# Performance work log

Measured on AMD Instinct MI355X. Metric: run time of the kernel, lower is better.

Reference implementation:

```python
import jax, jax.numpy as jnp
import numpy as np

N_CELLS = 2048
D_IN = 512
D_HID = 1024
D_OUT = 512
SYNC = 0.15
DEBATE = 0.15
N_FACTIONS = 8


def setup_inputs() -> dict:
    key = jax.random.key(0)
    ks = jax.random.split(key, 24)
    def w(k, shape, s=0.02):
        return jax.random.normal(k, shape, dtype=jnp.float32) * s
    ein = D_IN + D_HID          # complex-engine input dim (1536)
    gin = D_OUT + 1 + D_HID     # GRU gate input dim (1537)
    return {
        "x": jax.random.normal(ks[0], (1, D_IN), dtype=jnp.float32),
        "h_re": w(ks[1], (N_CELLS, D_HID), 0.1),
        "h_im": w(ks[2], (N_CELLS, D_HID), 0.1),
        "ea_wr": w(ks[3], (ein, D_OUT)), "ea_br": w(ks[4], (D_OUT,)),
        "ea_wi": w(ks[5], (ein, D_OUT)), "ea_bi": w(ks[6], (D_OUT,)),
        "eg_wr": w(ks[7], (ein, D_OUT)), "eg_br": w(ks[8], (D_OUT,)),
        "eg_wi": w(ks[9], (ein, D_OUT)), "eg_bi": w(ks[10], (D_OUT,)),
        "gz_w": w(ks[11], (gin, D_HID)), "gz_b": w(ks[12], (D_HID,)),
        "gr_w": w(ks[13], (gin, D_HID)), "gr_b": w(ks[14], (D_HID,)),
        "ghr_w": w(ks[15], (gin, D_HID)), "ghr_b": w(ks[16], (D_HID,)),
        "ghi_w": w(ks[17], (gin, D_HID)), "ghi_b": w(ks[18], (D_HID,)),
        "oh_w": w(ks[19], (2 * D_OUT, D_IN)), "oh_b": w(ks[20], (D_IN,)),
        "step": 7,
    }


def _clin(a, b, Wr, br, Wi, bi):
    # complex linear: (Wr + iWi)(a + ib) with torch's bias semantics
    return (a @ Wr + br) - (b @ Wi + bi), (b @ Wr + br) + (a @ Wi + bi)


def reference(x, h_re, h_im, ea_wr, ea_br, ea_wi, ea_bi, eg_wr, eg_br, eg_wi, eg_bi,
              gz_w, gz_b, gr_w, gr_b, ghr_w, ghr_b, ghi_w, ghi_b, oh_w, oh_b, step):
    # batch the 256-cell Python loop into single GEMMs over the cell axis
    xb = jnp.broadcast_to(x, (N_CELLS, D_IN))
    c_re = jnp.concatenate([xb, h_re], -1)                       # [N, D_IN+D_HID]
    c_im = jnp.concatenate([jnp.zeros_like(xb), h_im], -1)
    a_re, a_im = _clin(c_re, c_im, ea_wr, ea_br, ea_wi, ea_bi)
    g_re, g_im = _clin(c_re, c_im, eg_wr, eg_br, eg_wi, eg_bi)
    o_re, o_im = a_re - g_re, a_im - g_im                        # [N, D_OUT]
    tension = jnp.mean(o_re**2 + o_im**2, -1)                    # [N]

    # GRU memory update (detached input, matching output.detach())
    so_re = jax.lax.stop_gradient(o_re)
    so_im = jax.lax.stop_gradient(o_im)
    t_sg = jax.lax.stop_gradient(tension)
    mem_re = jnp.concatenate([so_re, t_sg[:, None]], -1)         # [N, D_OUT+1]
    mem_im = jnp.concatenate([so_im, jnp.zeros((N_CELLS, 1), o_im.dtype)], -1)
    x_mag = jnp.sqrt(mem_re**2 + mem_im**2)
    h_mag = jnp.sqrt(h_re**2 + h_im**2)
    cm = jnp.concatenate([x_mag, h_mag], -1)                     # [N, D_OUT+1+D_HID]
    z = jax.nn.sigmoid(cm @ gz_w + gz_b)
    r = jax.nn.sigmoid(cm @ gr_w + gr_b)
    comb_r = jnp.concatenate([mem_re, r * h_re], -1)
    comb_i = jnp.concatenate([mem_im, r * h_im], -1)
    cand_re = jnp.tanh(comb_r @ ghr_w + ghr_b)
    cand_im = jnp.tanh(comb_i @ ghi_w + ghi_b)
    nh_re = jax.lax.stop_gradient((1 - z) * h_re + z * cand_re)
    nh_im = jax.lax.stop_gradient((1 - z) * h_im + z * cand_im)

    # faction sync + debate (linear op, applied per component)
    fs = N_CELLS // N_FACTIONS
    def sync(h):
        hf = h.reshape(N_FACTIONS, fs, D_HID)
        hf = (1 - SYNC) * hf + SYNC * jnp.mean(hf, 1, keepdims=True)
        if step > 5:
            glob = jnp.mean(jnp.mean(hf, 1), 0)                  # [D_HID]
            dc = max(1, fs // 4)
            hf = hf.at[:, :dc].set((1 - DEBATE) * hf[:, :dc] + DEBATE * glob)
        return hf.reshape(N_CELLS, D_HID)
    nh_re, nh_im = sync(nh_re), sync(nh_im)

    # tension-softmax-weighted combination (weights are non-differentiable, .item() in torch)
    w_soft = jax.nn.softmax(t_sg)                                # [N]
    comb_re = (w_soft[:, None] * o_re).sum(0, keepdims=True)     # [1, D_OUT]
    comb_im = (w_soft[:, None] * o_im).sum(0, keepdims=True)
    out_real = jnp.concatenate([comb_re, comb_im], -1)           # [1, 2*D_OUT]
    pred = out_real @ oh_w + oh_b                                # [1, D_IN]
    return pred, jnp.mean(tension), nh_re, nh_im
```

## Files before the change

### kernel.cpp

```cpp
#include <hip/hip_runtime.h>
#include <math.h>

#define N_CELLS 2048
#define D_IN 512
#define D_HID 1024
#define D_OUT 512

typedef __attribute__((ext_vector_type(8))) short bf16x8;
typedef __attribute__((ext_vector_type(4))) float f32x4;
typedef __attribute__((ext_vector_type(4))) short short4v;

#define MFMA16(a, b, c) __builtin_amdgcn_mfma_f32_16x16x32_bf16(a, b, c, 0, 0, 0)

__device__ __forceinline__ short f2bf(float f) {
  union { float f; unsigned u; } v; v.f = f;
  unsigned r = (v.u + 0x7FFFu + ((v.u >> 16) & 1u)) >> 16;
  return (short)r;
}

__device__ __forceinline__ void gl_lds16(const void* g, void* l) {
  __builtin_amdgcn_global_load_lds(
      (const __attribute__((address_space(1))) void*)g,
      (__attribute__((address_space(3))) void*)l, 16, 0, 0);
}

__global__ __launch_bounds__(256) void k_transpose_all(
    const float* __restrict__ w0, const float* __restrict__ w1,
    const float* __restrict__ w2, const float* __restrict__ w3,
    short* __restrict__ t0, short* __restrict__ t1,
    short* __restrict__ t2, short* __restrict__ t3,
    const float* __restrict__ ea_wr, const float* __restrict__ eg_wr,
    const float* __restrict__ ea_wi, const float* __restrict__ eg_wi,
    short* __restrict__ wdrT, short* __restrict__ wdiT, short* __restrict__ wdnT) {
  const int k0 = blockIdx.x * 32, n0 = blockIdx.y * 32;
  const int c = threadIdx.x & 31, r4 = threadIdx.x >> 5;
  if (blockIdx.z < 4) {
    const float* w = (blockIdx.z == 0) ? w0 : (blockIdx.z == 1) ? w1
                   : (blockIdx.z == 2) ? w2 : w3;
    short* wT = (blockIdx.z == 0) ? t0 : (blockIdx.z == 1) ? t1
              : (blockIdx.z == 2) ? t2 : t3;
    __shared__ float t[32][33];
#pragma unroll
    for (int i = 0; i < 4; ++i) {
      int kl = r4 * 4 + i;
      int k = k0 + kl;
      int srcrow = (k < 512) ? k : k + 1;
      t[kl][c] = w[(size_t)srcrow * D_HID + n0 + c];
    }
    __syncthreads();
#pragma unroll
    for (int i = 0; i < 4; ++i) {
      int nl = r4 * 4 + i;
      wT[(size_t)(n0 + nl) * 1536 + k0 + c] = f2bf(t[c][nl]);
    }
  } else {
    if (blockIdx.x >= 32 || blockIdx.y >= 16) return;
    __shared__ float tr[32][33], ti[32][33];
#pragma unroll
    for (int i = 0; i < 4; ++i) {
      int kl = r4 * 4 + i;
      int src = (512 + k0 + kl) * D_OUT + n0 + c;
      tr[kl][c] = ea_wr[src] - eg_wr[src];
      ti[kl][c] = ea_wi[src] - eg_wi[src];
    }
    __syncthreads();
#pragma unroll
    for (int i = 0; i < 4; ++i) {
      int nl = r4 * 4 + i;
      int dst = (n0 + nl) * D_HID + k0 + c;
      float dr = tr[c][nl], di = ti[c][nl];
      wdrT[dst] = f2bf(dr);
      wdiT[dst] = f2bf(di);
      wdnT[dst] = f2bf(-di);
    }
  }
}

__global__ __launch_bounds__(256) void k_prep_h(
    const float* __restrict__ h_re, const float* __restrict__ h_im,
    short* __restrict__ hbre, short* __restrict__ hbim, short* __restrict__ gatesA,
    float* __restrict__ tens) {
  if (threadIdx.x == 0) tens[blockIdx.x] = 0.f;
  int idx4 = (blockIdx.x * 256 + threadIdx.x) * 4;
  int m = idx4 >> 10, n = idx4 & 1023;
  float4 hr = *(const float4*)&h_re[idx4];
  float4 hi = *(const float4*)&h_im[idx4];
  short4v br, bi, bm;
  br.x = f2bf(hr.x); br.y = f2bf(hr.y); br.z = f2bf(hr.z); br.w = f2bf(hr.w);
  bi.x = f2bf(hi.x); bi.y = f2bf(hi.y); bi.z = f2bf(hi.z); bi.w = f2bf(hi.w);
  bm.x = f2bf(sqrtf(hr.x * hr.x + hi.x * hi.x));
  bm.y = f2bf(sqrtf(hr.y * hr.y + hi.y * hi.y));
  bm.z = f2bf(sqrtf(hr.z * hr.z + hi.z * hi.z));
  bm.w = f2bf(sqrtf(hr.w * hr.w + hi.w * hi.w));
  *(short4v*)&hbre[idx4] = br;
  *(short4v*)&hbim[idx4] = bi;
  *(short4v*)&gatesA[(size_t)m * 1536 + 512 + n] = bm;
}

__global__ __launch_bounds__(256) void k_bias_part(
    const float* __restrict__ x,
    const float* __restrict__ ea_wr, const float* __restrict__ ea_wi,
    const float* __restrict__ eg_wr, const float* __restrict__ eg_wi,
    float* __restrict__ bpartr, float* __restrict__ bparti) {
  int n = blockIdx.x * 256 + threadIdx.x;
  int kc = blockIdx.y;
  float sr = 0.f, si = 0.f;
  for (int i = 0; i < 64; ++i) {
    int k = kc * 64 + i;
    float xv = x[k];
    int idx = k * D_OUT + n;
    sr += xv * (ea_wr[idx] - eg_wr[idx]);
    si += xv * (ea_wi[idx] - eg_wi[idx]);
  }
  bpartr[kc * D_OUT + n] = sr;
  bparti[kc * D_OUT + n] = si;
}

__global__ __launch_bounds__(256) void k_bias_red(
    const float* __restrict__ bpartr, const float* __restrict__ bparti,
    const float* __restrict__ ea_br, const float* __restrict__ ea_bi,
    const float* __restrict__ eg_br, const float* __restrict__ eg_bi,
    float* __restrict__ bias_re, float* __restrict__ bias_im) {
  int n = blockIdx.x * 256 + threadIdx.x;
  float sr = 0.f, si = 0.f;
#pragma unroll
  for (int kc = 0; kc < 8; ++kc) { sr += bpartr[kc * D_OUT + n]; si += bparti[kc * D_OUT + n]; }
  float brd = ea_br[n] - eg_br[n];
  float bid = ea_bi[n] - eg_bi[n];
  bias_re[n] = sr + brd - bid;
  bias_im[n] = si + brd + bid;
}

__global__ __launch_bounds__(256) void k_engine(
    const short* __restrict__ hbre, const short* __restrict__ hbim,
    const short* __restrict__ wdrT, const short* __restrict__ wdiT,
    const short* __restrict__ wdnT,
    const float* __restrict__ bias_re, const float* __restrict__ bias_im,
    float* __restrict__ ore, float* __restrict__ oim,
    short* __restrict__ gatesA, short* __restrict__ candAre, short* __restrict__ candAim,
    float* __restrict__ tens) {
  __shared__ short Ar[2 * 64 * 32], Ai[2 * 64 * 32];
  __shared__ short Brs[2 * 32 * 32], Bis[2 * 32 * 32], Bns[2 * 32 * 32];
  const int m0 = blockIdx.x * 64, n0 = blockIdx.y * 32;
  const int tid = threadIdx.x;
  const int wid = tid >> 6, lane = tid & 63;
  const int quad = lane >> 4, lcol = lane & 15;
  const int wm = wid * 16;
  f32x4 accre[2], accim[2];
#pragma unroll
  for (int nt = 0; nt < 2; ++nt) {
    accre[nt] = (f32x4){0.f, 0.f, 0.f, 0.f};
    accim[nt] = (f32x4){0.f, 0.f, 0.f, 0.f};
  }
  for (int k0 = 0; k0 < D_HID; k0 += 64) {
    if (k0) __syncthreads();
#pragma unroll
    for (int i = 0; i < 2; ++i) {
      int c = i * 256 + tid;
      int kh = c >> 8, row = (c >> 2) & 63, kq = c & 3;
      size_t g = (size_t)(m0 + row) * D_HID + k0 + kh * 32 + kq * 8;
      gl_lds16(hbre + g, &Ar[c * 8]);
      gl_lds16(hbim + g, &Ai[c * 8]);
    }
    {
      int c = tid;
      int kh = c >> 7, row = (c >> 2) & 31, kq = c & 3;
      size_t g = (size_t)(n0 + row) * D_HID + k0 + kh * 32 + kq * 8;
      gl_lds16(wdrT + g, &Brs[c * 8]);
      gl_lds16(wdiT + g, &Bis[c * 8]);
      gl_lds16(wdnT + g, &Bns[c * 8]);
    }
    __syncthreads();
#pragma unroll
    for (int kh = 0; kh < 2; ++kh) {
      bf16x8 ar, ai, br[2], bi[2], bn[2];
      int aoff = kh * 2048 + (wm + lcol) * 32 + quad * 8;
      ar = *(const bf16x8*)&Ar[aoff];
      ai = *(const bf16x8*)&Ai[aoff];
#pragma unroll
      for (int nt = 0; nt < 2; ++nt) {
        int boff = kh * 1024 + (nt * 16 + lcol) * 32 + quad * 8;
        br[nt] = *(const bf16x8*)&Brs[boff];
        bi[nt] = *(const bf16x8*)&Bis[boff];
        bn[nt] = *(const bf16x8*)&Bns[boff];
      }
#pragma unroll
      for (int nt = 0; nt < 2; ++nt) {
        accre[nt] = MFMA16(ar, br[nt], accre[nt]);
        accre[nt] = MFMA16(ai, bn[nt], accre[nt]);
        accim[nt] = MFMA16(ar, bi[nt], accim[nt]);
        accim[nt] = MFMA16(ai, br[nt], accim[nt]);
      }
    }
  }
#pragma unroll
  for (int r = 0; r < 4; ++r) {
    int m = m0 + wm + quad * 4 + r;
    float t = 0.f;
#pragma unroll
    for (int nt = 0; nt < 2; ++nt) {
      int n = n0 + nt * 16 + lcol;
      float cre = accre[nt][r] + bias_re[n];
      float cim = accim[nt][r] + bias_im[n];
      t += cre * cre + cim * cim;
      ore[(size_t)m * D_OUT + n] = cre;
      oim[(size_t)m * D_OUT + n] = cim;
      gatesA[(size_t)m * 1536 + n] = f2bf(sqrtf(cre * cre + cim * cim));
      candAre[(size_t)m * 1536 + n] = f2bf(cre);
      candAim[(size_t)m * 1536 + n] = f2bf(cim);
    }
#pragma unroll
    for (int off = 1; off < 16; off <<= 1) t += __shfl_xor(t, off);
    if (lcol == 0) atomicAdd(&tens[m], t * (1.f / 512.f));
  }
}

__global__ __launch_bounds__(256) void k_gates(
    const short* __restrict__ gatesA,
    const short* __restrict__ gzwT, const short* __restrict__ grwT,
    const float* __restrict__ gz_w, const float* __restrict__ gz_b,
    const float* __restrict__ gr_w, const float* __restrict__ gr_b,
    const float* __restrict__ tens,
    const float* __restrict__ h_re, const float* __restrict__ h_im,
    float* __restrict__ zbuf,
    short* __restrict__ candAre, short* __restrict__ candAim) {
  __shared__ short As[2 * 64 * 32];
  __shared__ short Bs[2 * 64 * 32];
  const int is_z = (blockIdx.z == 0);
  const short* Bt = is_z ? gzwT : grwT;
  const int m0 = blockIdx.x * 64, n0 = blockIdx.y * 64;
  const int tid = threadIdx.x;
  const int wid = tid >> 6, lane = tid & 63;
  const int quad = lane >> 4, lcol = lane & 15;
  const int wm = (wid >> 1) * 32, wn = (wid & 1) * 32;
  f32x4 acc[2][2];
#pragma unroll
  for (int mt = 0; mt < 2; ++mt)
#pragma unroll
    for (int nt = 0; nt < 2; ++nt) acc[mt][nt] = (f32x4){0.f, 0.f, 0.f, 0.f};
  for (int k0 = 0; k0 < 1536; k0 += 64) {
    if (k0) __syncthreads();
#pragma unroll
    for (int i = 0; i < 2; ++i) {
      int c = i * 256 + tid;
      int kh = c >> 8, row = (c >> 2) & 63, kq = c & 3;
      gl_lds16(gatesA + (size_t)(m0 + row) * 1536 + k0 + kh * 32 + kq * 8, &As[c * 8]);
      gl_lds16(Bt + (size_t)(n0 + row) * 1536 + k0 + kh * 32 + kq * 8, &Bs[c * 8]);
    }
    __syncthreads();
#pragma unroll
    for (int kh = 0; kh < 2; ++kh) {
      bf16x8 a[2], b[2];
#pragma unroll
      for (int mt = 0; mt < 2; ++mt)
        a[mt] = *(const bf16x8*)&As[kh * 2048 + (wm + mt * 16 + lcol) * 32 + quad * 8];
#pragma unroll
      for (int nt = 0; nt < 2; ++nt)
        b[nt] = *(const bf16x8*)&Bs[kh * 2048 + (wn + nt * 16 + lcol) * 32 + quad * 8];
#pragma unroll
      for (int mt = 0; mt < 2; ++mt)
#pragma unroll
        for (int nt = 0; nt < 2; ++nt)
          acc[mt][nt] = MFMA16(a[mt], b[nt], acc[mt][nt]);
    }
  }
#pragma unroll
  for (int mt = 0; mt < 2; ++mt)
#pragma unroll
    for (int nt = 0; nt < 2; ++nt)
#pragma unroll
      for (int r = 0; r < 4; ++r) {
        int m = m0 + wm + mt * 16 + quad * 4 + r;
        int n = n0 + wn + nt * 16 + lcol;
        float tv = tens[m];
        if (is_z) {
          float zp = acc[mt][nt][r] + gz_b[n] + tv * gz_w[(size_t)512 * D_HID + n];
          zbuf[(size_t)m * D_HID + n] = 1.f / (1.f + expf(-zp));
        } else {
          float rp = acc[mt][nt][r] + gr_b[n] + tv * gr_w[(size_t)512 * D_HID + n];
          float rr = 1.f / (1.f + expf(-rp));
          candAre[(size_t)m * 1536 + 512 + n] = f2bf(rr * h_re[(size_t)m * D_HID + n]);
          candAim[(size_t)m * 1536 + 512 + n] = f2bf(rr * h_im[(size_t)m * D_HID + n]);
        }
      }
}

__global__ __launch_bounds__(256) void k_cand(
    const short* __restrict__ candAre, const short* __restrict__ candAim,
    const short* __restrict__ ghrwT, const short* __restrict__ ghiwT,
    const float* __restrict__ ghr_b, const float* __restrict__ ghi_b,
    const float* __restrict__ ghr_w,
    const float* __restrict__ tens, const float* __restrict__ zbuf,
    const float* __restrict__ h_re, const float* __restrict__ h_im,
    float* __restrict__ nhre, float* __restrict__ nhim) {
  __shared__ short As[2 * 64 * 32];
  __shared__ short Bs[2 * 64 * 32];
  const int is_re = (blockIdx.z == 0);
  const short* A = is_re ? candAre : candAim;
  const short* Bt = is_re ? ghrwT : ghiwT;
  const float* bias = is_re ? ghr_b : ghi_b;
  const float* h = is_re ? h_re : h_im;
  float* outp = is_re ? nhre : nhim;
  const int m0 = blockIdx.x * 64, n0 = blockIdx.y * 64;
  const int tid = threadIdx.x;
  const int wid = tid >> 6, lane = tid & 63;
  const int quad = lane >> 4, lcol = lane & 15;
  const int wm = (wid >> 1) * 32, wn = (wid & 1) * 32;
  f32x4 acc[2][2];
#pragma unroll
  for (int mt = 0; mt < 2; ++mt)
#pragma unroll
    for (int nt = 0; nt < 2; ++nt) acc[mt][nt] = (f32x4){0.f, 0.f, 0.f, 0.f};
  for (int k0 = 0; k0 < 1536; k0 += 64) {
    if (k0) __syncthreads();
#pragma unroll
    for (int i = 0; i < 2; ++i) {
      int c = i * 256 + tid;
      int kh = c >> 8, row = (c >> 2) & 63, kq = c & 3;
      gl_lds16(A + (size_t)(m0 + row) * 1536 + k0 + kh * 32 + kq * 8, &As[c * 8]);
      gl_lds16(Bt + (size_t)(n0 + row) * 1536 + k0 + kh * 32 + kq * 8, &Bs[c * 8]);
    }
    __syncthreads();
#pragma unroll
    for (int kh = 0; kh < 2; ++kh) {
      bf16x8 a[2], b[2];
#pragma unroll
      for (int mt = 0; mt < 2; ++mt)
        a[mt] = *(const bf16x8*)&As[kh * 2048 + (wm + mt * 16 + lcol) * 32 + quad * 8];
#pragma unroll
      for (int nt = 0; nt < 2; ++nt)
        b[nt] = *(const bf16x8*)&Bs[kh * 2048 + (wn + nt * 16 + lcol) * 32 + quad * 8];
#pragma unroll
      for (int mt = 0; mt < 2; ++mt)
#pragma unroll
        for (int nt = 0; nt < 2; ++nt)
          acc[mt][nt] = MFMA16(a[mt], b[nt], acc[mt][nt]);
    }
  }
#pragma unroll
  for (int mt = 0; mt < 2; ++mt)
#pragma unroll
    for (int nt = 0; nt < 2; ++nt)
#pragma unroll
      for (int r = 0; r < 4; ++r) {
        int m = m0 + wm + mt * 16 + quad * 4 + r;
        int n = n0 + wn + nt * 16 + lcol;
        float pre = acc[mt][nt][r] + bias[n];
        if (is_re) pre += tens[m] * ghr_w[(size_t)512 * D_HID + n];
        float cand = tanhf(pre);
        float z = zbuf[(size_t)m * D_HID + n];
        float hv = h[(size_t)m * D_HID + n];
        outp[(size_t)m * D_HID + n] = (1.f - z) * hv + z * cand;
      }
}

__global__ __launch_bounds__(256) void k_fsum_part(
    const float* __restrict__ nhre, const float* __restrict__ nhim,
    float* __restrict__ fpart) {
  int f = blockIdx.x >> 3, rc = blockIdx.x & 7, comp = blockIdx.y;
  const float* src = comp ? nhim : nhre;
  int row0 = f * 256 + rc * 32;
#pragma unroll
  for (int nc = 0; nc < 4; ++nc) {
    int n = nc * 256 + threadIdx.x;
    float s = 0.f;
    const float* base = src + (size_t)row0 * D_HID + n;
    for (int j = 0; j < 32; ++j) s += base[(size_t)j * D_HID];
    fpart[((size_t)comp * 64 + blockIdx.x) * D_HID + n] = s;
  }
}

__global__ __launch_bounds__(256) void k_fsum_red(
    const float* __restrict__ fpart,
    float* __restrict__ fsre, float* __restrict__ fsim,
    float* __restrict__ gre, float* __restrict__ gim) {
  int n = blockIdx.x * 256 + threadIdx.x;
  int comp = blockIdx.y;
  float* fs = comp ? fsim : fsre;
  float* g = comp ? gim : gre;
  float gsum = 0.f;
#pragma unroll
  for (int f = 0; f < 8; ++f) {
    float sf = 0.f;
#pragma unroll
    for (int rc = 0; rc < 8; ++rc)
      sf += fpart[((size_t)comp * 64 + f * 8 + rc) * D_HID + n];
    fs[f * D_HID + n] = sf;
    gsum += sf;
  }
  g[n] = gsum * (1.f / 2048.f);
}

__global__ __launch_bounds__(256) void k_sync(
    float* __restrict__ nhre, float* __restrict__ nhim,
    const float* __restrict__ fsre, const float* __restrict__ fsim,
    const float* __restrict__ gre, const float* __restrict__ gim,
    const int* __restrict__ step) {
  int idx = blockIdx.x * 256 + threadIdx.x;
  int m = idx >> 10, n = idx & 1023;
  int f = m >> 8;
  float vr = nhre[idx], vi = nhim[idx];
  vr = 0.85f * vr + 0.15f * (fsre[f * D_HID + n] * (1.f / 256.f));
  vi = 0.85f * vi + 0.15f * (fsim[f * D_HID + n] * (1.f / 256.f));
  if (step[0] > 5 && (m & 255) < 64) {
    vr = 0.85f * vr + 0.15f * gre[n];
    vi = 0.85f * vi + 0.15f * gim[n];
  }
  nhre[idx] = vr;
  nhim[idx] = vi;
}

__global__ __launch_bounds__(1024) void k_stats(
    const float* __restrict__ tens, float* __restrict__ wsoft,
    float* __restrict__ meanT_out) {
  __shared__ float red[16];
  __shared__ float s_max, s_sum;
  int tid = threadIdx.x;
  int wid = tid >> 6, lane = tid & 63;
  float a = tens[tid], b = tens[tid + 1024];
  float mx = fmaxf(a, b);
  for (int off = 32; off; off >>= 1) mx = fmaxf(mx, __shfl_down(mx, off));
  if (lane == 0) red[wid] = mx;
  __syncthreads();
  if (tid == 0) {
    float m2 = red[0];
    for (int i = 1; i < 16; ++i) m2 = fmaxf(m2, red[i]);
    s_max = m2;
  }
  __syncthreads();
  float mxv = s_max;
  float ea = expf(a - mxv), eb = expf(b - mxv);
  float se = ea + eb;
  for (int off = 32; off; off >>= 1) se += __shfl_down(se, off);
  __syncthreads();
  if (lane == 0) red[wid] = se;
  __syncthreads();
  if (tid == 0) {
    float s2 = 0.f;
    for (int i = 0; i < 16; ++i) s2 += red[i];
    s_sum = s2;
  }
  __syncthreads();
  float inv = 1.f / s_sum;
  wsoft[tid] = ea * inv;
  wsoft[tid + 1024] = eb * inv;
  float st = a + b;
  for (int off = 32; off; off >>= 1) st += __shfl_down(st, off);
  __syncthreads();
  if (lane == 0) red[wid] = st;
  __syncthreads();
  if (tid == 0) {
    float s2 = 0.f;
    for (int i = 0; i < 16; ++i) s2 += red[i];
    meanT_out[0] = s2 * (1.f / 2048.f);
  }
}

__global__ __launch_bounds__(256) void k_comb_part(
    const float* __restrict__ ore, const float* __restrict__ oim,
    const float* __restrict__ wsoft, float* __restrict__ cpart) {
  int j = blockIdx.x * 256 + threadIdx.x;
  int mc = blockIdx.y;
  const float* src = (j < 512) ? ore : oim;
  int col = j & 511;
  float s = 0.f;
  for (int i = 0; i < 128; ++i) {
    int m = mc * 128 + i;
    s += wsoft[m] * src[(size_t)m * D_OUT + col];
  }
  cpart[(size_t)mc * 1024 + j] = s;
}

__global__ __launch_bounds__(256) void k_pred_part(
    const float* __restrict__ cpart, const float* __restrict__ oh_w,
    float* __restrict__ ppart) {
  __shared__ float combs[128];
  int tid = threadIdx.x;
  int jc = blockIdx.y;
  if (tid < 128) {
    float s = 0.f;
#pragma unroll
    for (int mc = 0; mc < 16; ++mc) s += cpart[(size_t)mc * 1024 + jc * 128 + tid];
    combs[tid] = s;
  }
  __syncthreads();
  int n = blockIdx.x * 256 + tid;
  float s = 0.f;
  for (int i = 0; i < 128; ++i)
    s += combs[i] * oh_w[(size_t)(jc * 128 + i) * D_IN + n];
  ppart[(size_t)jc * D_IN + n] = s;
}

__global__ __launch_bounds__(256) void k_pred_red(
    const float* __restrict__ ppart, const float* __restrict__ oh_b,
    float* __restrict__ pred) {
  int n = blockIdx.x * 256 + threadIdx.x;
  float s = oh_b[n];
#pragma unroll
  for (int jc = 0; jc < 8; ++jc) s += ppart[(size_t)jc * D_IN + n];
  pred[n] = s;
}

extern "C" void kernel_launch(void* const* d_in, const int* in_sizes, int n_in,
                              void* d_out, int out_size, void* d_ws, size_t ws_size,
                              hipStream_t stream) {
  const float* x     = (const float*)d_in[0];
  const float* h_re  = (const float*)d_in[1];
  const float* h_im  = (const float*)d_in[2];
  const float* ea_wr = (const float*)d_in[3];
  const float* ea_br = (const float*)d_in[4];
  const float* ea_wi = (const float*)d_in[5];
  const float* ea_bi = (const float*)d_in[6];
  const float* eg_wr = (const float*)d_in[7];
  const float* eg_br = (const float*)d_in[8];
  const float* eg_wi = (const float*)d_in[9];
  const float* eg_bi = (const float*)d_in[10];
  const float* gz_w  = (const float*)d_in[11];
  const float* gz_b  = (const float*)d_in[12];
  const float* gr_w  = (const float*)d_in[13];
  const float* gr_b  = (const float*)d_in[14];
  const float* ghr_w = (const float*)d_in[15];
  const float* ghr_b = (const float*)d_in[16];
  const float* ghi_w = (const float*)d_in[17];
  const float* ghi_b = (const float*)d_in[18];
  const float* oh_w  = (const float*)d_in[19];
  const float* oh_b  = (const float*)d_in[20];
  const int*   step  = (const int*)d_in[21];

  float* out = (float*)d_out;
  float* pred_out  = out;
  float* meanT_out = out + 512;
  float* nhre_out  = out + 513;
  float* nhim_out  = out + 513 + N_CELLS * D_HID;

  char* p = (char*)d_ws;
  auto carve = [&](size_t bytes) { char* r = p; p += (bytes + 255) & ~(size_t)255; return r; };
  short* wdrT   = (short*)carve(512 * 1024 * 2);
  short* wdiT   = (short*)carve(512 * 1024 * 2);
  short* wdnT   = (short*)carve(512 * 1024 * 2);
  short* gzwT   = (short*)carve(1024 * 1536 * 2);
  short* grwT   = (short*)carve(1024 * 1536 * 2);
  short* ghrwT  = (short*)carve(1024 * 1536 * 2);
  short* ghiwT  = (short*)carve(1024 * 1536 * 2);
  short* hbre   = (short*)carve(2048 * 1024 * 2);
  short* hbim   = (short*)carve(2048 * 1024 * 2);
  short* gatesA = (short*)carve((size_t)2048 * 1536 * 2);
  short* candAre= (short*)carve((size_t)2048 * 1536 * 2);
  short* candAim= (short*)carve((size_t)2048 * 1536 * 2);
  float* ore    = (float*)carve(2048 * 512 * 4);
  float* oim    = (float*)carve(2048 * 512 * 4);
  float* zbuf   = (float*)carve((size_t)2048 * 1024 * 4);
  float* bias_re= (float*)carve(512 * 4);
  float* bias_im= (float*)carve(512 * 4);
  float* bpartr = (float*)carve(8 * 512 * 4);
  float* bparti = (float*)carve(8 * 512 * 4);
  float* tens   = (float*)carve(2048 * 4);
  float* fpart  = (float*)carve(2 * 64 * 1024 * 4);
  float* fsre   = (float*)carve(8 * 1024 * 4);
  float* fsim   = (float*)carve(8 * 1024 * 4);
  float* gre    = (float*)carve(1024 * 4);
  float* gim    = (float*)carve(1024 * 4);
  float* wsoft  = (float*)carve(2048 * 4);
  float* cpart  = (float*)carve(16 * 1024 * 4);
  float* ppart  = (float*)carve(8 * 512 * 4);

  hipLaunchKernelGGL(k_transpose_all, dim3(48, 32, 5), dim3(256), 0, stream,
                     gz_w, gr_w, ghr_w, ghi_w, gzwT, grwT, ghrwT, ghiwT,
                     ea_wr, eg_wr, ea_wi, eg_wi, wdrT, wdiT, wdnT);
  hipLaunchKernelGGL(k_prep_h, dim3(2048), dim3(256), 0, stream,
                     h_re, h_im, hbre, hbim, gatesA, tens);
  hipLaunchKernelGGL(k_bias_part, dim3(2, 8), dim3(256), 0, stream,
                     x, ea_wr, ea_wi, eg_wr, eg_wi, bpartr, bparti);
  hipLaunchKernelGGL(k_bias_red, dim3(2), dim3(256), 0, stream,
                     bpartr, bparti, ea_br, ea_bi, eg_br, eg_bi, bias_re, bias_im);
  hipLaunchKernelGGL(k_engine, dim3(32, 16), dim3(256), 0, stream,
                     hbre, hbim, wdrT, wdiT, wdnT, bias_re, bias_im,
                     ore, oim, gatesA, candAre, candAim, tens);
  hipLaunchKernelGGL(k_gates, dim3(32, 16, 2), dim3(256), 0, stream,
                     gatesA, gzwT, grwT, gz_w, gz_b, gr_w, gr_b, tens,
                     h_re, h_im, zbuf, candAre, candAim);
  hipLaunchKernelGGL(k_cand, dim3(32, 16, 2), dim3(256), 0, stream,
                     candAre, candAim, ghrwT, ghiwT, ghr_b, ghi_b, ghr_w,
                     tens, zbuf, h_re, h_im, nhre_out, nhim_out);
  hipLaunchKernelGGL(k_fsum_part, dim3(64, 2), dim3(256), 0, stream,
                     nhre_out, nhim_out, fpart);
  hipLaunchKernelGGL(k_fsum_red, dim3(4, 2), dim3(256), 0, stream,
                     fpart, fsre, fsim, gre, gim);
  hipLaunchKernelGGL(k_sync, dim3((N_CELLS * D_HID) / 256), dim3(256), 0, stream,
                     nhre_out, nhim_out, fsre, fsim, gre, gim, step);
  hipLaunchKernelGGL(k_stats, dim3(1), dim3(1024), 0, stream, tens, wsoft, meanT_out);
  hipLaunchKernelGGL(k_comb_part, dim3(4, 16), dim3(256), 0, stream,
                     ore, oim, wsoft, cpart);
  hipLaunchKernelGGL(k_pred_part, dim3(2, 8), dim3(256), 0, stream, cpart, oh_w, ppart);
  hipLaunchKernelGGL(k_pred_red, dim3(2), dim3(256), 0, stream, ppart, oh_b, pred_out);
}
```

Measured before the change: 277.3 us.

## Merge prep kernels, double-buffer GEMM LDS, bf16 z buffer, atomic faction sums

```diff
diff --git a/kernel.cpp b/kernel.cpp
--- a/kernel.cpp
+++ b/kernel.cpp
@@ -18,171 +18,171 @@
   return (short)r;
 }
 
+__device__ __forceinline__ float bf2f(unsigned short u) {
+  union { unsigned u; float f; } v; v.u = ((unsigned)u) << 16; return v.f;
+}
+
 __device__ __forceinline__ void gl_lds16(const void* g, void* l) {
   __builtin_amdgcn_global_load_lds(
       (const __attribute__((address_space(1))) void*)g,
       (__attribute__((address_space(3))) void*)l, 16, 0, 0);
 }
 
-__global__ __launch_bounds__(256) void k_transpose_all(
+__global__ __launch_bounds__(256) void k_prep_all(
     const float* __restrict__ w0, const float* __restrict__ w1,
     const float* __restrict__ w2, const float* __restrict__ w3,
     short* __restrict__ t0, short* __restrict__ t1,
     short* __restrict__ t2, short* __restrict__ t3,
     const float* __restrict__ ea_wr, const float* __restrict__ eg_wr,
     const float* __restrict__ ea_wi, const float* __restrict__ eg_wi,
-    short* __restrict__ wdrT, short* __restrict__ wdiT, short* __restrict__ wdnT) {
-  const int k0 = blockIdx.x * 32, n0 = blockIdx.y * 32;
-  const int c = threadIdx.x & 31, r4 = threadIdx.x >> 5;
-  if (blockIdx.z < 4) {
-    const float* w = (blockIdx.z == 0) ? w0 : (blockIdx.z == 1) ? w1
-                   : (blockIdx.z == 2) ? w2 : w3;
-    short* wT = (blockIdx.z == 0) ? t0 : (blockIdx.z == 1) ? t1
-              : (blockIdx.z == 2) ? t2 : t3;
-    __shared__ float t[32][33];
+    short* __restrict__ wdrT, short* __restrict__ wdiT, short* __restrict__ wdnT,
+    const float* __restrict__ h_re, const float* __restrict__ h_im,
+    short* __restrict__ hbre, short* __restrict__ hbim, short* __restrict__ gatesA,
+    float* __restrict__ tens,
+    const float* __restrict__ x,
+    float* __restrict__ bpartr, float* __restrict__ bparti,
+    float* __restrict__ fsbuf) {
+  __shared__ float ts0[32][33], ts1[32][33];
+  const int z = blockIdx.z;
+  const int bx = blockIdx.x;
+  const int tid = threadIdx.x;
+  if (z < 4) {
+    if (bx >= 1536) return;
+    const int xx = bx % 48, yy = bx / 48;
+    const float* w = (z == 0) ? w0 : (z == 1) ? w1 : (z == 2) ? w2 : w3;
+    short* wT = (z == 0) ? t0 : (z == 1) ? t1 : (z == 2) ? t2 : t3;
+    const int k0 = xx * 32, n0 = yy * 32;
+    const int c = tid & 31, r4 = tid >> 5;
 #pragma unroll
     for (int i = 0; i < 4; ++i) {
       int kl = r4 * 4 + i;
       int k = k0 + kl;
       int srcrow = (k < 512) ? k : k + 1;
-      t[kl][c] = w[(size_t)srcrow * D_HID + n0 + c];
+      ts0[kl][c] = w[(size_t)srcrow * D_HID + n0 + c];
     }
     __syncthreads();
 #pragma unroll
     for (int i = 0; i < 4; ++i) {
       int nl = r4 * 4 + i;
-      wT[(size_t)(n0 + nl) * 1536 + k0 + c] = f2bf(t[c][nl]);
-    }
-  } else {
-    if (blockIdx.x >= 32 || blockIdx.y >= 16) return;
-    __shared__ float tr[32][33], ti[32][33];
+      wT[(size_t)(n0 + nl) * 1536 + k0 + c] = f2bf(ts0[c][nl]);
+    }
+  } else if (z == 4) {
+    const int xx = bx % 48, yy = bx / 48;
+    if (xx >= 32 || yy >= 16) return;
+    const int k0 = xx * 32, n0 = yy * 32;
+    const int c = tid & 31, r4 = tid >> 5;
 #pragma unroll
     for (int i = 0; i < 4; ++i) {
       int kl = r4 * 4 + i;
       int src = (512 + k0 + kl) * D_OUT + n0 + c;
-      tr[kl][c] = ea_wr[src] - eg_wr[src];
-      ti[kl][c] = ea_wi[src] - eg_wi[src];
+      ts0[kl][c] = ea_wr[src] - eg_wr[src];
+      ts1[kl][c] = ea_wi[src] - eg_wi[src];
     }
     __syncthreads();
 #pragma unroll
     for (int i = 0; i < 4; ++i) {
       int nl = r4 * 4 + i;
       int dst = (n0 + nl) * D_HID + k0 + c;
-      float dr = tr[c][nl], di = ti[c][nl];
+      float dr = ts0[c][nl], di = ts1[c][nl];
       wdrT[dst] = f2bf(dr);
       wdiT[dst] = f2bf(di);
       wdnT[dst] = f2bf(-di);
     }
-  }
-}
-
-__global__ __launch_bounds__(256) void k_prep_h(
-    const float* __restrict__ h_re, const float* __restrict__ h_im,
-    short* __restrict__ hbre, short* __restrict__ hbim, short* __restrict__ gatesA,
-    float* __restrict__ tens) {
-  if (threadIdx.x == 0) tens[blockIdx.x] = 0.f;
-  int idx4 = (blockIdx.x * 256 + threadIdx.x) * 4;
-  int m = idx4 >> 10, n = idx4 & 1023;
-  float4 hr = *(const float4*)&h_re[idx4];
-  float4 hi = *(const float4*)&h_im[idx4];
-  short4v br, bi, bm;
-  br.x = f2bf(hr.x); br.y = f2bf(hr.y); br.z = f2bf(hr.z); br.w = f2bf(hr.w);
-  bi.x = f2bf(hi.x); bi.y = f2bf(hi.y); bi.z = f2bf(hi.z); bi.w = f2bf(hi.w);
-  bm.x = f2bf(sqrtf(hr.x * hr.x + hi.x * hi.x));
-  bm.y = f2bf(sqrtf(hr.y * hr.y + hi.y * hi.y));
-  bm.z = f2bf(sqrtf(hr.z * hr.z + hi.z * hi.z));
-  bm.w = f2bf(sqrtf(hr.w * hr.w + hi.w * hi.w));
-  *(short4v*)&hbre[idx4] = br;
-  *(short4v*)&hbim[idx4] = bi;
-  *(short4v*)&gatesA[(size_t)m * 1536 + 512 + n] = bm;
-}
-
-__global__ __launch_bounds__(256) void k_bias_part(
-    const float* __restrict__ x,
-    const float* __restrict__ ea_wr, const float* __restrict__ ea_wi,
-    const float* __restrict__ eg_wr, const float* __restrict__ eg_wi,
-    float* __restrict__ bpartr, float* __restrict__ bparti) {
-  int n = blockIdx.x * 256 + threadIdx.x;
-  int kc = blockIdx.y;
-  float sr = 0.f, si = 0.f;
-  for (int i = 0; i < 64; ++i) {
-    int k = kc * 64 + i;
-    float xv = x[k];
-    int idx = k * D_OUT + n;
-    sr += xv * (ea_wr[idx] - eg_wr[idx]);
-    si += xv * (ea_wi[idx] - eg_wi[idx]);
-  }
-  bpartr[kc * D_OUT + n] = sr;
-  bparti[kc * D_OUT + n] = si;
-}
-
-__global__ __launch_bounds__(256) void k_bias_red(
-    const float* __restrict__ bpartr, const float* __restrict__ bparti,
-    const float* __restrict__ ea_br, const float* __restrict__ ea_bi,
-    const float* __restrict__ eg_br, const float* __restrict__ eg_bi,
-    float* __restrict__ bias_re, float* __restrict__ bias_im) {
-  int n = blockIdx.x * 256 + threadIdx.x;
-  float sr = 0.f, si = 0.f;
-#pragma unroll
-  for (int kc = 0; kc < 8; ++kc) { sr += bpartr[kc * D_OUT + n]; si += bparti[kc * D_OUT + n]; }
-  float brd = ea_br[n] - eg_br[n];
-  float bid = ea_bi[n] - eg_bi[n];
-  bias_re[n] = sr + brd - bid;
-  bias_im[n] = si + brd + bid;
+  } else if (z == 5) {
+    if (tid == 0) tens[bx] = 0.f;
+    int idx4 = (bx * 256 + tid) * 4;
+    int m = idx4 >> 10, n = idx4 & 1023;
+    float4 hr = *(const float4*)&h_re[idx4];
+    float4 hi = *(const float4*)&h_im[idx4];
+    short4v br, bi, bm;
+    br.x = f2bf(hr.x); br.y = f2bf(hr.y); br.z = f2bf(hr.z); br.w = f2bf(hr.w);
+    bi.x = f2bf(hi.x); bi.y = f2bf(hi.y); bi.z = f2bf(hi.z); bi.w = f2bf(hi.w);
+    bm.x = f2bf(sqrtf(hr.x * hr.x + hi.x * hi.x));
+    bm.y = f2bf(sqrtf(hr.y * hr.y + hi.y * hi.y));
+    bm.z = f2bf(sqrtf(hr.z * hr.z + hi.z * hi.z));
+    bm.w = f2bf(sqrtf(hr.w * hr.w + hi.w * hi.w));
+    *(short4v*)&hbre[idx4] = br;
+    *(short4v*)&hbim[idx4] = bi;
+    *(short4v*)&gatesA[(size_t)m * 1536 + 512 + n] = bm;
+  } else {
+    if (bx < 16) {
+      int n = (bx & 1) * 256 + tid;
+      int kc = bx >> 1;
+      float sr = 0.f, si = 0.f;
+      for (int i = 0; i < 64; ++i) {
+        int k = kc * 64 + i;
+        float xv = x[k];
+        int idx = k * D_OUT + n;
+        sr += xv * (ea_wr[idx] - eg_wr[idx]);
+        si += xv * (ea_wi[idx] - eg_wi[idx]);
+      }
+      bpartr[kc * D_OUT + n] = sr;
+      bparti[kc * D_OUT + n] = si;
+    } else if (bx < 32) {
+      int i = (bx - 16) * 1024 + tid * 4;
+      *(float4*)&fsbuf[i] = (float4){0.f, 0.f, 0.f, 0.f};
+    }
+  }
 }
 
 __global__ __launch_bounds__(256) void k_engine(
     const short* __restrict__ hbre, const short* __restrict__ hbim,
     const short* __restrict__ wdrT, const short* __restrict__ wdiT,
     const short* __restrict__ wdnT,
-    const float* __restrict__ bias_re, const float* __restrict__ bias_im,
+    const float* __restrict__ bpartr, const float* __restrict__ bparti,
+    const float* __restrict__ ea_br, const float* __restrict__ ea_bi,
+    const float* __restrict__ eg_br, const float* __restrict__ eg_bi,
     float* __restrict__ ore, float* __restrict__ oim,
     short* __restrict__ gatesA, short* __restrict__ candAre, short* __restrict__ candAim,
     float* __restrict__ tens) {
-  __shared__ short Ar[2 * 64 * 32], Ai[2 * 64 * 32];
-  __shared__ short Brs[2 * 32 * 32], Bis[2 * 32 * 32], Bns[2 * 32 * 32];
+  __shared__ short Ar[2][4096], Ai[2][4096];
+  __shared__ short Brs[2][2048], Bis[2][2048], Bns[2][2048];
   const int m0 = blockIdx.x * 64, n0 = blockIdx.y * 32;
   const int tid = threadIdx.x;
   const int wid = tid >> 6, lane = tid & 63;
   const int quad = lane >> 4, lcol = lane & 15;
   const int wm = wid * 16;
-  f32x4 accre[2], accim[2];
-#pragma unroll
-  for (int nt = 0; nt < 2; ++nt) {
-    accre[nt] = (f32x4){0.f, 0.f, 0.f, 0.f};
-    accim[nt] = (f32x4){0.f, 0.f, 0.f, 0.f};
-  }
-  for (int k0 = 0; k0 < D_HID; k0 += 64) {
-    if (k0) __syncthreads();
+  auto stage = [&](int buf, int k0) {
 #pragma unroll
     for (int i = 0; i < 2; ++i) {
       int c = i * 256 + tid;
       int kh = c >> 8, row = (c >> 2) & 63, kq = c & 3;
       size_t g = (size_t)(m0 + row) * D_HID + k0 + kh * 32 + kq * 8;
-      gl_lds16(hbre + g, &Ar[c * 8]);
-      gl_lds16(hbim + g, &Ai[c * 8]);
+      gl_lds16(hbre + g, &Ar[buf][c * 8]);
+      gl_lds16(hbim + g, &Ai[buf][c * 8]);
     }
     {
       int c = tid;
       int kh = c >> 7, row = (c >> 2) & 31, kq = c & 3;
       size_t g = (size_t)(n0 + row) * D_HID + k0 + kh * 32 + kq * 8;
-      gl_lds16(wdrT + g, &Brs[c * 8]);
-      gl_lds16(wdiT + g, &Bis[c * 8]);
-      gl_lds16(wdnT + g, &Bns[c * 8]);
-    }
+      gl_lds16(wdrT + g, &Brs[buf][c * 8]);
+      gl_lds16(wdiT + g, &Bis[buf][c * 8]);
+      gl_lds16(wdnT + g, &Bns[buf][c * 8]);
+    }
+  };
+  f32x4 accre[2], accim[2];
+#pragma unroll
+  for (int nt = 0; nt < 2; ++nt) {
+    accre[nt] = (f32x4){0.f, 0.f, 0.f, 0.f};
+    accim[nt] = (f32x4){0.f, 0.f, 0.f, 0.f};
+  }
+  stage(0, 0);
+  for (int kt = 0; kt < 16; ++kt) {
     __syncthreads();
+    if (kt < 15) stage((kt & 1) ^ 1, (kt + 1) * 64);
+    const int buf = kt & 1;
 #pragma unroll
     for (int kh = 0; kh < 2; ++kh) {
       bf16x8 ar, ai, br[2], bi[2], bn[2];
       int aoff = kh * 2048 + (wm + lcol) * 32 + quad * 8;
-      ar = *(const bf16x8*)&Ar[aoff];
-      ai = *(const bf16x8*)&Ai[aoff];
+      ar = *(const bf16x8*)&Ar[buf][aoff];
+      ai = *(const bf16x8*)&Ai[buf][aoff];
 #pragma unroll
       for (int nt = 0; nt < 2; ++nt) {
         int boff = kh * 1024 + (nt * 16 + lcol) * 32 + quad * 8;
-        br[nt] = *(const bf16x8*)&Brs[boff];
-        bi[nt] = *(const bf16x8*)&Bis[boff];
-        bn[nt] = *(const bf16x8*)&Bns[boff];
+        br[nt] = *(const bf16x8*)&Brs[buf][boff];
+        bi[nt] = *(const bf16x8*)&Bis[buf][boff];
+        bn[nt] = *(const bf16x8*)&Bns[buf][boff];
       }
 #pragma unroll
       for (int nt = 0; nt < 2; ++nt) {
@@ -193,6 +193,18 @@
       }
     }
   }
+  float biasre[2], biasim[2];
+#pragma unroll
+  for (int nt = 0; nt < 2; ++nt) {
+    int n = n0 + nt * 16 + lcol;
+    float sr = 0.f, si = 0.f;
+#pragma unroll
+    for (int kc = 0; kc < 8; ++kc) { sr += bpartr[kc * D_OUT + n]; si += bparti[kc * D_OUT + n]; }
+    float brd = ea_br[n] - eg_br[n];
+    float bid = ea_bi[n] - eg_bi[n];
+    biasre[nt] = sr + brd - bid;
+    biasim[nt] = si + brd + bid;
+  }
 #pragma unroll
   for (int r = 0; r < 4; ++r) {
     int m = m0 + wm + quad * 4 + r;
@@ -200,8 +212,8 @@
 #pragma unroll
     for (int nt = 0; nt < 2; ++nt) {
       int n = n0 + nt * 16 + lcol;
-      float cre = accre[nt][r] + bias_re[n];
-      float cim = accim[nt][r] + bias_im[n];
+      float cre = accre[nt][r] + biasre[nt];
+      float cim = accim[nt][r] + biasim[nt];
       t += cre * cre + cim * cim;
       ore[(size_t)m * D_OUT + n] = cre;
       oim[(size_t)m * D_OUT + n] = cim;
@@ -222,10 +234,10 @@
     const float* __restrict__ gr_w, const float* __restrict__ gr_b,
     const float* __restrict__ tens,
     const float* __restrict__ h_re, const float* __restrict__ h_im,
-    float* __restrict__ zbuf,
+    unsigned short* __restrict__ zbuf,
     short* __restrict__ candAre, short* __restrict__ candAim) {
-  __shared__ short As[2 * 64 * 32];
-  __shared__ short Bs[2 * 64 * 32];
+  __shared__ short As[2][4096];
+  __shared__ short Bs[2][4096];
   const int is_z = (blockIdx.z == 0);
   const short* Bt = is_z ? gzwT : grwT;
   const int m0 = blockIdx.x * 64, n0 = blockIdx.y * 64;
@@ -233,30 +245,34 @@
   const int wid = tid >> 6, lane = tid & 63;
   const int quad = lane >> 4, lcol = lane & 15;
   const int wm = (wid >> 1) * 32, wn = (wid & 1) * 32;
-  f32x4 acc[2][2];
-#pragma unroll
-  for (int mt = 0; mt < 2; ++mt)
-#pragma unroll
-    for (int nt = 0; nt < 2; ++nt) acc[mt][nt] = (f32x4){0.f, 0.f, 0.f, 0.f};
-  for (int k0 = 0; k0 < 1536; k0 += 64) {
-    if (k0) __syncthreads();
+  auto stage = [&](int buf, int k0) {
 #pragma unroll
     for (int i = 0; i < 2; ++i) {
       int c = i * 256 + tid;
       int kh = c >> 8, row = (c >> 2) & 63, kq = c & 3;
-      gl_lds16(gatesA + (size_t)(m0 + row) * 1536 + k0 + kh * 32 + kq * 8, &As[c * 8]);
-      gl_lds16(Bt + (size_t)(n0 + row) * 1536 + k0 + kh * 32 + kq * 8, &Bs[c * 8]);
-    }
+      gl_lds16(gatesA + (size_t)(m0 + row) * 1536 + k0 + kh * 32 + kq * 8, &As[buf][c * 8]);
+      gl_lds16(Bt + (size_t)(n0 + row) * 1536 + k0 + kh * 32 + kq * 8, &Bs[buf][c * 8]);
+    }
+  };
+  f32x4 acc[2][2];
+#pragma unroll
+  for (int mt = 0; mt < 2; ++mt)
+#pragma unroll
+    for (int nt = 0; nt < 2; ++nt) acc[mt][nt] = (f32x4){0.f, 0.f, 0.f, 0.f};
+  stage(0, 0);
+  for (int kt = 0; kt < 24; ++kt) {
     __syncthreads();
+    if (kt < 23) stage((kt & 1) ^ 1, (kt + 1) * 64);
+    const int buf = kt & 1;
 #pragma unroll
     for (int kh = 0; kh < 2; ++kh) {
       bf16x8 a[2], b[2];
 #pragma unroll
       for (int mt = 0; mt < 2; ++mt)
-        a[mt] = *(const bf16x8*)&As[kh * 2048 + (wm + mt * 16 + lcol) * 32 + quad * 8];
+        a[mt] = *(const bf16x8*)&As[buf][kh * 2048 + (wm + mt * 16 + lcol) * 32 + quad * 8];
 #pragma unroll
       for (int nt = 0; nt < 2; ++nt)
-        b[nt] = *(const bf16x8*)&Bs[kh * 2048 + (wn + nt * 16 + lcol) * 32 + quad * 8];
+        b[nt] = *(const bf16x8*)&Bs[buf][kh * 2048 + (wn + nt * 16 + lcol) * 32 + quad * 8];
 #pragma unroll
       for (int mt = 0; mt < 2; ++mt)
 #pragma unroll
@@ -275,7 +291,7 @@
         float tv = tens[m];
         if (is_z) {
           float zp = acc[mt][nt][r] + gz_b[n] + tv * gz_w[(size_t)512 * D_HID + n];
-          zbuf[(size_t)m * D_HID + n] = 1.f / (1.f + expf(-zp));
+          zbuf[(size_t)m * D_HID + n] = (unsigned short)f2bf(1.f / (1.f + expf(-zp)));
         } else {
           float rp = acc[mt][nt][r] + gr_b[n] + tv * gr_w[(size_t)512 * D_HID + n];
           float rr = 1.f / (1.f + expf(-rp));
@@ -290,11 +306,11 @@
     const short* __restrict__ ghrwT, const short* __restrict__ ghiwT,
     const float* __restrict__ ghr_b, const float* __restrict__ ghi_b,
     const float* __restrict__ ghr_w,
-    const float* __restrict__ tens, const float* __restrict__ zbuf,
+    const float* __restrict__ tens, const unsigned short* __restrict__ zbuf,
     const float* __restrict__ h_re, const float* __restrict__ h_im,
     float* __restrict__ nhre, float* __restrict__ nhim) {
-  __shared__ short As[2 * 64 * 32];
-  __shared__ short Bs[2 * 64 * 32];
+  __shared__ short As[2][4096];
+  __shared__ short Bs[2][4096];
   const int is_re = (blockIdx.z == 0);
   const short* A = is_re ? candAre : candAim;
   const short* Bt = is_re ? ghrwT : ghiwT;
@@ -306,30 +322,34 @@
   const int wid = tid >> 6, lane = tid & 63;
   const int quad = lane >> 4, lcol = lane & 15;
   const int wm = (wid >> 1) * 32, wn = (wid & 1) * 32;
-  f32x4 acc[2][2];
-#pragma unroll
-  for (int mt = 0; mt < 2; ++mt)
-#pragma unroll
-    for (int nt = 0; nt < 2; ++nt) acc[mt][nt] = (f32x4){0.f, 0.f, 0.f, 0.f};
-  for (int k0 = 0; k0 < 1536; k0 += 64) {
-    if (k0) __syncthreads();
+  auto stage = [&](int buf, int k0) {
 #pragma unroll
     for (int i = 0; i < 2; ++i) {
       int c = i * 256 + tid;
       int kh = c >> 8, row = (c >> 2) & 63, kq = c & 3;
-      gl_lds16(A + (size_t)(m0 + row) * 1536 + k0 + kh * 32 + kq * 8, &As[c * 8]);
-      gl_lds16(Bt + (size_t)(n0 + row) * 1536 + k0 + kh * 32 + kq * 8, &Bs[c * 8]);
-    }
+      gl_lds16(A + (size_t)(m0 + row) * 1536 + k0 + kh * 32 + kq * 8, &As[buf][c * 8]);
+      gl_lds16(Bt + (size_t)(n0 + row) * 1536 + k0 + kh * 32 + kq * 8, &Bs[buf][c * 8]);
+    }
+  };
+  f32x4 acc[2][2];
+#pragma unroll
+  for (int mt = 0; mt < 2; ++mt)
+#pragma unroll
+    for (int nt = 0; nt < 2; ++nt) acc[mt][nt] = (f32x4){0.f, 0.f, 0.f, 0.f};
+  stage(0, 0);
+  for (int kt = 0; kt < 24; ++kt) {
     __syncthreads();
+    if (kt < 23) stage((kt & 1) ^ 1, (kt + 1) * 64);
+    const int buf = kt & 1;
 #pragma unroll
     for (int kh = 0; kh < 2; ++kh) {
       bf16x8 a[2], b[2];
 #pragma unroll
       for (int mt = 0; mt < 2; ++mt)
-        a[mt] = *(const bf16x8*)&As[kh * 2048 + (wm + mt * 16 + lcol) * 32 + quad * 8];
+        a[mt] = *(const bf16x8*)&As[buf][kh * 2048 + (wm + mt * 16 + lcol) * 32 + quad * 8];
 #pragma unroll
       for (int nt = 0; nt < 2; ++nt)
-        b[nt] = *(const bf16x8*)&Bs[kh * 2048 + (wn + nt * 16 + lcol) * 32 + quad * 8];
+        b[nt] = *(const bf16x8*)&Bs[buf][kh * 2048 + (wn + nt * 16 + lcol) * 32 + quad * 8];
 #pragma unroll
       for (int mt = 0; mt < 2; ++mt)
 #pragma unroll
@@ -348,7 +368,7 @@
         float pre = acc[mt][nt][r] + bias[n];
         if (is_re) pre += tens[m] * ghr_w[(size_t)512 * D_HID + n];
         float cand = tanhf(pre);
-        float z = zbuf[(size_t)m * D_HID + n];
+        float z = bf2f(zbuf[(size_t)m * D_HID + n]);
         float hv = h[(size_t)m * D_HID + n];
         outp[(size_t)m * D_HID + n] = (1.f - z) * hv + z * cand;
       }
@@ -356,9 +376,10 @@
 
 __global__ __launch_bounds__(256) void k_fsum_part(
     const float* __restrict__ nhre, const float* __restrict__ nhim,
-    float* __restrict__ fpart) {
+    float* __restrict__ fsbuf) {
   int f = blockIdx.x >> 3, rc = blockIdx.x & 7, comp = blockIdx.y;
   const float* src = comp ? nhim : nhre;
+  float* fs = fsbuf + (size_t)comp * 8192;
   int row0 = f * 256 + rc * 32;
 #pragma unroll
   for (int nc = 0; nc < 4; ++nc) {
@@ -366,45 +387,28 @@
     float s = 0.f;
     const float* base = src + (size_t)row0 * D_HID + n;
     for (int j = 0; j < 32; ++j) s += base[(size_t)j * D_HID];
-    fpart[((size_t)comp * 64 + blockIdx.x) * D_HID + n] = s;
-  }
-}
-
-__global__ __launch_bounds__(256) void k_fsum_red(
-    const float* __restrict__ fpart,
-    float* __restrict__ fsre, float* __restrict__ fsim,
-    float* __restrict__ gre, float* __restrict__ gim) {
-  int n = blockIdx.x * 256 + threadIdx.x;
-  int comp = blockIdx.y;
-  float* fs = comp ? fsim : fsre;
-  float* g = comp ? gim : gre;
-  float gsum = 0.f;
-#pragma unroll
-  for (int f = 0; f < 8; ++f) {
-    float sf = 0.f;
-#pragma unroll
-    for (int rc = 0; rc < 8; ++rc)
-      sf += fpart[((size_t)comp * 64 + f * 8 + rc) * D_HID + n];
-    fs[f * D_HID + n] = sf;
-    gsum += sf;
-  }
-  g[n] = gsum * (1.f / 2048.f);
+    atomicAdd(&fs[(size_t)n * 8 + f], s);
+  }
 }
 
 __global__ __launch_bounds__(256) void k_sync(
     float* __restrict__ nhre, float* __restrict__ nhim,
-    const float* __restrict__ fsre, const float* __restrict__ fsim,
-    const float* __restrict__ gre, const float* __restrict__ gim,
-    const int* __restrict__ step) {
+    const float* __restrict__ fsbuf, const int* __restrict__ step) {
   int idx = blockIdx.x * 256 + threadIdx.x;
   int m = idx >> 10, n = idx & 1023;
   int f = m >> 8;
+  const float* f0 = fsbuf + (size_t)n * 8;
+  const float* f1 = fsbuf + 8192 + (size_t)n * 8;
+  float gr = 0.f, gi = 0.f;
+#pragma unroll
+  for (int ff = 0; ff < 8; ++ff) { gr += f0[ff]; gi += f1[ff]; }
+  float fr = f0[f], fi = f1[f];
   float vr = nhre[idx], vi = nhim[idx];
-  vr = 0.85f * vr + 0.15f * (fsre[f * D_HID + n] * (1.f / 256.f));
-  vi = 0.85f * vi + 0.15f * (fsim[f * D_HID + n] * (1.f / 256.f));
+  vr = 0.85f * vr + 0.15f * (fr * (1.f / 256.f));
+  vi = 0.85f * vi + 0.15f * (fi * (1.f / 256.f));
   if (step[0] > 5 && (m & 255) < 64) {
-    vr = 0.85f * vr + 0.15f * gre[n];
-    vi = 0.85f * vi + 0.15f * gim[n];
+    vr = 0.85f * vr + 0.15f * (gr * (1.f / 2048.f));
+    vi = 0.85f * vi + 0.15f * (gi * (1.f / 2048.f));
   }
   nhre[idx] = vr;
   nhim[idx] = vi;
@@ -549,32 +553,23 @@
   short* candAim= (short*)carve((size_t)2048 * 1536 * 2);
   float* ore    = (float*)carve(2048 * 512 * 4);
   float* oim    = (float*)carve(2048 * 512 * 4);
-  float* zbuf   = (float*)carve((size_t)2048 * 1024 * 4);
-  float* bias_re= (float*)carve(512 * 4);
-  float* bias_im= (float*)carve(512 * 4);
+  unsigned short* zbuf = (unsigned short*)carve((size_t)2048 * 1024 * 2);
   float* bpartr = (float*)carve(8 * 512 * 4);
   float* bparti = (float*)carve(8 * 512 * 4);
   float* tens   = (float*)carve(2048 * 4);
-  float* fpart  = (float*)carve(2 * 64 * 1024 * 4);
-  float* fsre   = (float*)carve(8 * 1024 * 4);
-  float* fsim   = (float*)carve(8 * 1024 * 4);
-  float* gre    = (float*)carve(1024 * 4);
-  float* gim    = (float*)carve(1024 * 4);
+  float* fsbuf  = (float*)carve(2 * 8192 * 4);
   float* wsoft  = (float*)carve(2048 * 4);
   float* cpart  = (float*)carve(16 * 1024 * 4);
   float* ppart  = (float*)carve(8 * 512 * 4);
 
-  hipLaunchKernelGGL(k_transpose_all, dim3(48, 32, 5), dim3(256), 0, stream,
+  hipLaunchKernelGGL(k_prep_all, dim3(2048, 1, 7), dim3(256), 0, stream,
                      gz_w, gr_w, ghr_w, ghi_w, gzwT, grwT, ghrwT, ghiwT,
-                     ea_wr, eg_wr, ea_wi, eg_wi, wdrT, wdiT, wdnT);
-  hipLaunchKernelGGL(k_prep_h, dim3(2048), dim3(256), 0, stream,
-                     h_re, h_im, hbre, hbim, gatesA, tens);
-  hipLaunchKernelGGL(k_bias_part, dim3(2, 8), dim3(256), 0, stream,
-                     x, ea_wr, ea_wi, eg_wr, eg_wi, bpartr, bparti);
-  hipLaunchKernelGGL(k_bias_red, dim3(2), dim3(256), 0, stream,
-                     bpartr, bparti, ea_br, ea_bi, eg_br, eg_bi, bias_re, bias_im);
+                     ea_wr, eg_wr, ea_wi, eg_wi, wdrT, wdiT, wdnT,
+                     h_re, h_im, hbre, hbim, gatesA, tens,
+                     x, bpartr, bparti, fsbuf);
   hipLaunchKernelGGL(k_engine, dim3(32, 16), dim3(256), 0, stream,
-                     hbre, hbim, wdrT, wdiT, wdnT, bias_re, bias_im,
+                     hbre, hbim, wdrT, wdiT, wdnT,
+                     bpartr, bparti, ea_br, ea_bi, eg_br, eg_bi,
                      ore, oim, gatesA, candAre, candAim, tens);
   hipLaunchKernelGGL(k_gates, dim3(32, 16, 2), dim3(256), 0, stream,
                      gatesA, gzwT, grwT, gz_w, gz_b, gr_w, gr_b, tens,
@@ -583,11 +578,9 @@
                      candAre, candAim, ghrwT, ghiwT, ghr_b, ghi_b, ghr_w,
                      tens, zbuf, h_re, h_im, nhre_out, nhim_out);
   hipLaunchKernelGGL(k_fsum_part, dim3(64, 2), dim3(256), 0, stream,
-                     nhre_out, nhim_out, fpart);
-  hipLaunchKernelGGL(k_fsum_red, dim3(4, 2), dim3(256), 0, stream,
-                     fpart, fsre, fsim, gre, gim);
+                     nhre_out, nhim_out, fsbuf);
   hipLaunchKernelGGL(k_sync, dim3((N_CELLS * D_HID) / 256), dim3(256), 0, stream,
-                     nhre_out, nhim_out, fsre, fsim, gre, gim, step);
+                     nhre_out, nhim_out, fsbuf, step);
   hipLaunchKernelGGL(k_stats, dim3(1), dim3(1024), 0, stream, tens, wsoft, meanT_out);
   hipLaunchKernelGGL(k_comb_part, dim3(4, 16), dim3(256), 0, stream,
                      ore, oim, wsoft, cpart);
```

After: 290.9 us. 1.05x slower.
